# Optimization experiments

Measured on AMD Instinct MI355X. Metric: run time of the kernel, lower is better.

Reference implementation:

```python
import jax, jax.numpy as jnp
import numpy as np

N = 100000   # nodes
E = 1600000  # directed edges
D_IN, D_HID, D_OUT, N_CLS = 128, 256, 128, 10
EPS = 1e-5


def gcn_conv(x, W, b, src, dst, n):
    # PyG GCNConv: h = XW, add self loops, sym-normalize, scatter-add to dst, + bias
    h = x @ W
    loop = jnp.arange(n)
    src_f = jnp.concatenate([src, loop])
    dst_f = jnp.concatenate([dst, loop])
    deg = jax.ops.segment_sum(jnp.ones(src_f.shape[0], h.dtype), dst_f, num_segments=n)
    dinv = jnp.where(deg > 0, jax.lax.rsqrt(deg), jnp.zeros_like(deg))
    norm = dinv[src_f] * dinv[dst_f]                    # [E+N]
    out = jax.ops.segment_sum(h[src_f] * norm[:, None], dst_f, num_segments=n)
    return out + b


def batchnorm(x, gamma, beta):
    # training-mode BatchNorm1d (batch statistics, biased variance)
    mu = x.mean(0)
    var = x.var(0)
    return gamma * (x - mu) * jax.lax.rsqrt(var + EPS) + beta


def setup_inputs() -> dict:
    key = jax.random.key(0)
    ks = jax.random.split(key, 12)
    x = jax.random.normal(ks[0], (N, D_IN), jnp.float32)
    edge_index = jax.random.randint(ks[1], (2, E), 0, N, dtype=jnp.int64)
    def lin(k, fi, fo):
        s = 1.0 / np.sqrt(fi)
        return jax.random.uniform(k, (fi, fo), jnp.float32, -s, s)
    return {
        "x": x, "edge_index": edge_index,
        "W1": lin(ks[2], D_IN, D_HID), "b1": jnp.zeros(D_HID, jnp.float32),
        "g1": jnp.ones(D_HID, jnp.float32), "beta1": jnp.zeros(D_HID, jnp.float32),
        "W2": lin(ks[3], D_HID, D_HID), "b2": jnp.zeros(D_HID, jnp.float32),
        "g2": jnp.ones(D_HID, jnp.float32), "beta2": jnp.zeros(D_HID, jnp.float32),
        "W3": lin(ks[4], D_HID, D_OUT), "b3": jnp.zeros(D_OUT, jnp.float32),
        "g3": jnp.ones(D_OUT, jnp.float32), "beta3": jnp.zeros(D_OUT, jnp.float32),
        "Wout": lin(ks[5], D_OUT, N_CLS), "bout": jnp.zeros(N_CLS, jnp.float32),
    }


def reference(x, edge_index, W1, b1, g1, beta1, W2, b2, g2, beta2,
              W3, b3, g3, beta3, Wout, bout):
    src, dst = edge_index[0], edge_index[1]
    h = jax.nn.relu(batchnorm(gcn_conv(x, W1, b1, src, dst, N), g1, beta1))
    h = jax.nn.relu(batchnorm(gcn_conv(h, W2, b2, src, dst, N), g2, beta2))
    h = jax.nn.relu(batchnorm(gcn_conv(h, W3, b3, src, dst, N), g3, beta3))
    return h @ Wout + bout
```

## Files before the change

### kernel.cpp

```cpp
#include <hip/hip_runtime.h>
#include <hip/hip_fp16.h>
#include <cstdint>
#include <cstddef>

#define EPS_BN 1e-5f
#define NSLICE 16

static inline int cdiv(int a, int b) { return (a + b - 1) / b; }

using half8   = __attribute__((ext_vector_type(8))) _Float16;
using floatx4 = __attribute__((ext_vector_type(4))) float;

__device__ __forceinline__ float atomAddF(float* p, float v) {
    return unsafeAtomicAdd(p, v);
}


__global__ __launch_bounds__(256) void k_hist(const int* __restrict__ dst, int E,
                                              int NBLK, int NBUCK, int* __restrict__ H) {
    __shared__ int h[256];
    int t = threadIdx.x;
    h[t] = 0;
    __syncthreads();
    int base = blockIdx.x * 4096;
#pragma unroll
    for (int j = 0; j < 16; ++j) {
        int e = base + j * 256 + t;
        if (e < E) atomicAdd(&h[dst[e] >> 9], 1);
    }
    __syncthreads();
    if (t < NBUCK) H[t * NBLK + blockIdx.x] = h[t];
}

__global__ __launch_bounds__(256) void k_scan_reduce(const int* __restrict__ in, int m,
                                                     int* __restrict__ bsum) {
    int base = blockIdx.x * 1024;
    int t = threadIdx.x;
    int s = 0;
#pragma unroll
    for (int i = 0; i < 4; ++i) {
        int idx = base + t * 4 + i;
        if (idx < m) s += in[idx];
    }
    __shared__ int sm[256];
    sm[t] = s;
    __syncthreads();
    for (int off = 128; off > 0; off >>= 1) {
        if (t < off) sm[t] += sm[t + off];
        __syncthreads();
    }
    if (t == 0) bsum[blockIdx.x] = sm[0];
}

__global__ void k_scan_bsum(int* __restrict__ bsum, int nb) {
    if (threadIdx.x == 0 && blockIdx.x == 0) {
        int acc = 0;
        for (int i = 0; i < nb; ++i) { int v = bsum[i]; bsum[i] = acc; acc += v; }
    }
}

__global__ __launch_bounds__(256) void k_scan_final(const int* __restrict__ in, int m,
                                                    const int* __restrict__ bsum,
                                                    int* __restrict__ outS) {
    int base = blockIdx.x * 1024;
    int t = threadIdx.x;
    int v[4];
    int s = 0;
#pragma unroll
    for (int i = 0; i < 4; ++i) {
        int idx = base + t * 4 + i;
        v[i] = (idx < m) ? in[idx] : 0;
        s += v[i];
    }
    __shared__ int sm[256];
    sm[t] = s;
    __syncthreads();
    for (int off = 1; off < 256; off <<= 1) {
        int x = (t >= off) ? sm[t - off] : 0;
        __syncthreads();
        sm[t] += x;
        __syncthreads();
    }
    int excl = sm[t] - s + bsum[blockIdx.x];
#pragma unroll
    for (int i = 0; i < 4; ++i) {
        int idx = base + t * 4 + i;
        if (idx < m) { outS[idx] = excl; excl += v[i]; }
    }
}

__global__ __launch_bounds__(256) void k_bucket(const int* __restrict__ src,
                                                const int* __restrict__ dst, int E,
                                                int NBLK, int NBUCK,
                                                const int* __restrict__ S,
                                                unsigned* __restrict__ pairs) {
    __shared__ int cur[256];
    int t = threadIdx.x;
    if (t < NBUCK) cur[t] = S[t * NBLK + blockIdx.x];
    __syncthreads();
    int base = blockIdx.x * 4096;
#pragma unroll
    for (int j = 0; j < 16; ++j) {
        int e = base + j * 256 + t;
        if (e < E) {
            unsigned s = (unsigned)src[e];
            unsigned d = (unsigned)dst[e];
            int p = atomicAdd(&cur[d >> 9], 1);
            pairs[p] = ((d & 511u) << 17) | s;
        }
    }
}

__global__ __launch_bounds__(256) void k_build(const unsigned* __restrict__ pairs,
                                               const int* __restrict__ S,
                                               int NBLK, int NBUCK, int n, int E,
                                               int* __restrict__ endoff,
                                               float* __restrict__ dinv,
                                               int* __restrict__ csr) {
    int b = blockIdx.x;
    int nbase = b << 9;
    int bstart = S[b * NBLK];
    int bend = (b == NBUCK - 1) ? E : S[(b + 1) * NBLK];
    int t = threadIdx.x;
    __shared__ int sdeg[512];
    __shared__ int scur[512];
    __shared__ int stmp[256];
    sdeg[t] = 0; sdeg[t + 256] = 0;
    __syncthreads();
    for (int e = bstart + t; e < bend; e += 256)
        atomicAdd(&sdeg[pairs[e] >> 17], 1);
    __syncthreads();
    int d0 = sdeg[2 * t], d1 = sdeg[2 * t + 1];
    int ps = d0 + d1;
    stmp[t] = ps;
    __syncthreads();
    for (int off = 1; off < 256; off <<= 1) {
        int x = (t >= off) ? stmp[t - off] : 0;
        __syncthreads();
        stmp[t] += x;
        __syncthreads();
    }
    int c0 = bstart + stmp[t] - ps;
    int c1 = c0 + d0;
    scur[2 * t] = c0;
    scur[2 * t + 1] = c1;
    int v0 = nbase + 2 * t, v1 = v0 + 1;
    if (v0 < n) { endoff[v0] = c1;      dinv[v0] = rsqrtf((float)(d0 + 1)); }
    if (v1 < n) { endoff[v1] = c1 + d1; dinv[v1] = rsqrtf((float)(d1 + 1)); }
    __syncthreads();
    for (int e = bstart + t; e < bend; e += 256) {
        unsigned p = pairs[e];
        int pos = atomicAdd(&scur[p >> 17], 1);
        csr[pos] = (int)(p & 0x1FFFFu);
    }
}

__global__ __launch_bounds__(256) void k_wtall(const float* __restrict__ W1,
                                               const float* __restrict__ W2,
                                               const float* __restrict__ W3,
                                               __half* __restrict__ Wt1,
                                               __half* __restrict__ Wt2,
                                               __half* __restrict__ Wt3) {
    int idx = blockIdx.x * 256 + threadIdx.x;
    if (idx < 32768) {
        int k = idx >> 8, c = idx & 255;
        Wt1[c * 128 + k] = __float2half(W1[idx]);
    } else if (idx < 98304) {
        int r = idx - 32768;
        int k = r >> 8, c = r & 255;
        Wt2[c * 256 + k] = __float2half(W2[r]);
    } else if (idx < 131072) {
        int r = idx - 98304;
        int k = r >> 7, c = r & 127;
        Wt3[c * 256 + k] = __float2half(W3[r]);
    }
}

__global__ __launch_bounds__(256) void k_x2h(const float* __restrict__ x,
                                             const float* __restrict__ dinv,
                                             __half* __restrict__ xh, int n) {
    int idx = blockIdx.x * 256 + threadIdx.x;
    int total = n * 16;
    if (idx >= total) return;
    int row = idx >> 4;
    float dv = dinv[row];
    const float4* p = (const float4*)x + (size_t)idx * 2;
    float4 a = p[0], b = p[1];
    uint4 o; __half2* oh = (__half2*)&o;
    oh[0] = __floats2half2_rn(a.x * dv, a.y * dv);
    oh[1] = __floats2half2_rn(a.z * dv, a.w * dv);
    oh[2] = __floats2half2_rn(b.x * dv, b.y * dv);
    oh[3] = __floats2half2_rn(b.z * dv, b.w * dv);
    ((uint4*)xh)[idx] = o;
}

__device__ __forceinline__ void acc8(float* acc, uint4 d) {
    const __half2* h = (const __half2*)&d;
#pragma unroll
    for (int j = 0; j < 4; ++j) {
        float2 f = __half22float2(h[j]);
        acc[2 * j] += f.x; acc[2 * j + 1] += f.y;
    }
}

template<int D, bool STATS>
__global__ __launch_bounds__(256) void k_gather_h(const int* __restrict__ csr,
                                                  const int* __restrict__ endoff,
                                                  const __half* __restrict__ P,
                                                  const float* __restrict__ dinv,
                                                  __half* __restrict__ S, int n,
                                                  float* __restrict__ sums,
                                                  float* __restrict__ sqs) {
    constexpr int LPN = D / 8;
    constexpr int NPB = 256 / LPN;
    __shared__ float red[STATS ? 2048 : 1];
    int t = threadIdx.x;
    int lane = t % LPN;
    int sub = t / LPN;
    float sacc[8] = {}, sqacc[8] = {};
    for (int vb = blockIdx.x * NPB; vb < n; vb += gridDim.x * NPB) {
        int v = vb + sub;
        if (v >= n) continue;
        int beg = (v == 0) ? 0 : endoff[v - 1];
        int end = endoff[v];
        float acc[8];
        {
            uint4 d = *((const uint4*)(P + (size_t)v * D) + lane);
            const __half2* h = (const __half2*)&d;
#pragma unroll
            for (int j = 0; j < 4; ++j) {
                float2 f = __half22float2(h[j]);
                acc[2 * j] = f.x; acc[2 * j + 1] = f.y;
            }
        }
        int i = beg;
        int rem = (end - beg) & 7;
        if (rem & 4) {
            uint4 dd[4];
#pragma unroll
            for (int u = 0; u < 4; ++u)
                dd[u] = *((const uint4*)(P + (size_t)csr[i + u] * D) + lane);
#pragma unroll
            for (int u = 0; u < 4; ++u) acc8(acc, dd[u]);
            i += 4;
        }
        if (rem & 2) {
            uint4 d0 = *((const uint4*)(P + (size_t)csr[i] * D) + lane);
            uint4 d1 = *((const uint4*)(P + (size_t)csr[i + 1] * D) + lane);
            acc8(acc, d0); acc8(acc, d1);
            i += 2;
        }
        if (rem & 1) {
            uint4 d0 = *((const uint4*)(P + (size_t)csr[i] * D) + lane);
            acc8(acc, d0);
            i += 1;
        }
        if (i < end) {
            uint4 a[8];
#pragma unroll
            for (int u = 0; u < 8; ++u)
                a[u] = *((const uint4*)(P + (size_t)csr[i + u] * D) + lane);
            for (i += 8; i < end; i += 8) {
                uint4 b[8];
#pragma unroll
                for (int u = 0; u < 8; ++u)
                    b[u] = *((const uint4*)(P + (size_t)csr[i + u] * D) + lane);
#pragma unroll
                for (int u = 0; u < 8; ++u) acc8(acc, a[u]);
#pragma unroll
                for (int u = 0; u < 8; ++u) a[u] = b[u];
            }
#pragma unroll
            for (int u = 0; u < 8; ++u) acc8(acc, a[u]);
        }
        float dv = dinv[v];
        uint4 o; __half2* oh = (__half2*)&o;
#pragma unroll
        for (int j = 0; j < 4; ++j) {
            float a0 = acc[2 * j] * dv, a1 = acc[2 * j + 1] * dv;
            oh[j] = __floats2half2_rn(a0, a1);
            if (STATS) {
                sacc[2 * j] += a0;  sqacc[2 * j] += a0 * a0;
                sacc[2 * j + 1] += a1; sqacc[2 * j + 1] += a1 * a1;
            }
        }
        *((uint4*)(S + (size_t)v * D) + lane) = o;
    }
    if (STATS) {
        int slice = blockIdx.x & (NSLICE - 1);
#pragma unroll
        for (int j = 0; j < 8; ++j) red[t * 8 + j] = sacc[j];
        __syncthreads();
        if (t < D) {
            int lc = t >> 3, j = t & 7;
            float ts = 0.f;
#pragma unroll
            for (int s = 0; s < NPB; ++s) ts += red[(s * LPN + lc) * 8 + j];
            atomAddF(&sums[slice * 256 + t], ts);
        }
        __syncthreads();
#pragma unroll
        for (int j = 0; j < 8; ++j) red[t * 8 + j] = sqacc[j];
        __syncthreads();
        if (t < D) {
            int lc = t >> 3, j = t & 7;
            float tq = 0.f;
#pragma unroll
            for (int s = 0; s < NPB; ++s) tq += red[(s * LPN + lc) * 8 + j];
            atomAddF(&sqs[slice * 256 + t], tq);
        }
    }
}

template<int K, int NC, bool SCALE, bool BNIN, bool STATS>
__global__ __launch_bounds__(256) void k_gemm_mfma(const __half* __restrict__ A,
                                                   const __half* __restrict__ Wt,
                                                   const float* __restrict__ dinv,
                                                   const float* __restrict__ isum,
                                                   const float* __restrict__ isq,
                                                   const float* __restrict__ g,
                                                   const float* __restrict__ beta,
                                                   float* __restrict__ osum,
                                                   float* __restrict__ osq,
                                                   __half* __restrict__ C, int n) {
    constexpr int LDA = 40;
    __shared__ _Float16 As[128 * LDA];
    __shared__ _Float16 Bs[128 * LDA];
    __shared__ float ssc[BNIN ? K : 1];
    __shared__ float ssh[BNIN ? K : 1];
    __shared__ float scs[STATS ? 128 : 1];
    __shared__ float scq[STATS ? 128 : 1];
    int tid = threadIdx.x;
    if (BNIN) {
        float nf = (float)n;
        for (int i = tid; i < K; i += 256) {
            float su = 0.f, sq = 0.f;
#pragma unroll
            for (int s = 0; s < NSLICE; ++s) {
                su += isum[s * 256 + i];
                sq += isq[s * 256 + i];
            }
            float mu = su / nf;
            float var = sq / nf - mu * mu;
            float sc = g[i] * rsqrtf(var + EPS_BN);
            ssc[i] = sc; ssh[i] = beta[i] - mu * sc;
        }
        __syncthreads();
    }
    int wave = tid >> 6, lane = tid & 63;
    int q = lane >> 4, l16 = lane & 15;
    int row0 = blockIdx.x * 128;
    int col0 = blockIdx.y * 128;
    floatx4 acc[2][8];
#pragma unroll
    for (int r = 0; r < 2; ++r)
#pragma unroll
        for (int c = 0; c < 8; ++c) acc[r][c] = (floatx4)0.0f;

    for (int k0 = 0; k0 < K; k0 += 32) {
#pragma unroll
        for (int i = 0; i < 2; ++i) {
            int s = tid + i * 256;
            int r = s >> 2, ks = s & 3;
            uint4 d = *(const uint4*)(A + (size_t)(row0 + r) * K + k0 + ks * 8);
            if (BNIN) {
                const __half2* h = (const __half2*)&d;
                uint4 o; __half2* oh = (__half2*)&o;
                int kb = k0 + ks * 8;
#pragma unroll
                for (int j = 0; j < 4; ++j) {
                    float2 f = __half22float2(h[j]);
                    float y0 = fmaxf(0.f, f.x * ssc[kb + 2 * j]     + ssh[kb + 2 * j]);
                    float y1 = fmaxf(0.f, f.y * ssc[kb + 2 * j + 1] + ssh[kb + 2 * j + 1]);
                    oh[j] = __floats2half2_rn(y0, y1);
                }
                d = o;
            }
            *(uint4*)&As[r * LDA + ks * 8] = d;
        }
#pragma unroll
        for (int i = 0; i < 2; ++i) {
            int s = tid + i * 256;
            int r = s >> 2, ks = s & 3;
            uint4 d = *(const uint4*)(Wt + (size_t)(col0 + r) * K + k0 + ks * 8);
            *(uint4*)&Bs[r * LDA + ks * 8] = d;
        }
        __syncthreads();
        half8 bf[8];
#pragma unroll
        for (int c = 0; c < 8; ++c)
            bf[c] = *(const half8*)&Bs[(c * 16 + l16) * LDA + q * 8];
#pragma unroll
        for (int r = 0; r < 2; ++r) {
            half8 af = *(const half8*)&As[(wave * 32 + r * 16 + l16) * LDA + q * 8];
#pragma unroll
            for (int c = 0; c < 8; ++c)
                acc[r][c] = __builtin_amdgcn_mfma_f32_16x16x32_f16(af, bf[c], acc[r][c], 0, 0, 0);
        }
        __syncthreads();
    }
    float colsum[8] = {};
    float colsq[8]  = {};
#pragma unroll
    for (int r = 0; r < 2; ++r) {
#pragma unroll
        for (int reg = 0; reg < 4; ++reg) {
            int grow = row0 + wave * 32 + r * 16 + q * 4 + reg;
            float sc = 1.f;
            if (SCALE) sc = (grow < n) ? dinv[grow] : 0.f;
            __half* cp = C + (size_t)grow * NC + col0 + l16;
#pragma unroll
            for (int c = 0; c < 8; ++c) {
                float v = acc[r][c][reg] * sc;
                cp[c * 16] = __float2half(v);
                if (STATS && grow < n) { colsum[c] += v; colsq[c] += v * v; }
            }
        }
    }
    if (STATS) {
        if (tid < 128) { scs[tid] = 0.f; scq[tid] = 0.f; }
        __syncthreads();
#pragma unroll
        for (int c = 0; c < 8; ++c) {
            atomicAdd(&scs[c * 16 + l16], colsum[c]);
            atomicAdd(&scq[c * 16 + l16], colsq[c]);
        }
        __syncthreads();
        if (tid < 128) {
            int slice = blockIdx.x & (NSLICE - 1);
            atomAddF(&osum[slice * 256 + col0 + tid], scs[tid]);
            atomAddF(&osq[slice * 256 + col0 + tid], scq[tid]);
        }
    }
}

__global__ __launch_bounds__(256) void k_out(const __half* __restrict__ H,
                                             const float* __restrict__ sums,
                                             const float* __restrict__ sqs,
                                             const float* __restrict__ g,
                                             const float* __restrict__ beta,
                                             const float* __restrict__ Wout,
                                             const float* __restrict__ bout,
                                             float* __restrict__ out, int n) {
    __shared__ float Wl[128 * 10];
    __shared__ float bl[10];
    __shared__ float osc[128];
    __shared__ float osh[128];
    __shared__ float red[64 * 40];
    int tid = threadIdx.x;
    for (int i = tid; i < 1280; i += 256) Wl[i] = Wout[i];
    if (tid < 10) bl[tid] = bout[tid];
    if (tid < 128) {
        float nf = (float)n;
        float su = 0.f, sq = 0.f;
#pragma unroll
        for (int s = 0; s < NSLICE; ++s) {
            su += sums[s * 256 + tid];
            sq += sqs[s * 256 + tid];
        }
        float mu = su / nf;
        float var = sq / nf - mu * mu;
        float sc = g[tid] * rsqrtf(var + EPS_BN);
        osc[tid] = sc; osh[tid] = beta[tid] - mu * sc;
    }
    __syncthreads();
    int rl = tid >> 2;
    int q = tid & 3;
    int r = blockIdx.x * 64 + rl;
    float p[10] = {};
    if (r < n) {
        const __half* a = H + (size_t)r * 128 + q * 32;
#pragma unroll 8
        for (int k = 0; k < 32; ++k) {
            int col = q * 32 + k;
            float av = fmaxf(0.f, __half2float(a[k]) * osc[col] + osh[col]);
            const float* wr = Wl + col * 10;
#pragma unroll
            for (int c = 0; c < 10; ++c) p[c] += av * wr[c];
        }
    }
    float* rr = red + (size_t)(rl * 4 + q) * 10;
#pragma unroll
    for (int c = 0; c < 10; ++c) rr[c] = p[c];
    __syncthreads();
    if (q == 0 && r < n) {
        const float* rb = red + (size_t)rl * 40;
#pragma unroll
        for (int c = 0; c < 10; ++c) {
            out[(size_t)r * 10 + c] = rb[c] + rb[10 + c] + rb[20 + c] + rb[30 + c] + bl[c];
        }
    }
}

extern "C" void kernel_launch(void* const* d_in, const int* in_sizes, int n_in,
                              void* d_out, int out_size, void* d_ws, size_t ws_size,
                              hipStream_t stream) {
    const float* x    = (const float*)d_in[0];
    const int*   ei   = (const int*)d_in[1];
    const float* W1   = (const float*)d_in[2];
    const float* g1   = (const float*)d_in[4];
    const float* be1  = (const float*)d_in[5];
    const float* W2   = (const float*)d_in[6];
    const float* g2   = (const float*)d_in[8];
    const float* be2  = (const float*)d_in[9];
    const float* W3   = (const float*)d_in[10];
    const float* g3   = (const float*)d_in[12];
    const float* be3  = (const float*)d_in[13];
    const float* Wout = (const float*)d_in[14];
    const float* bout = (const float*)d_in[15];
    float* out = (float*)d_out;

    int n = in_sizes[0] / 128;
    int E = in_sizes[1] / 2;
    const int* esrc = ei;
    const int* edst = ei + E;
    int npad = cdiv(n, 128) * 128;
    int NBLK = cdiv(E, 4096);
    int NBUCK = (n + 511) >> 9;
    if (NBUCK > 256) return;
    int m = NBUCK * NBLK;
    int nb2 = cdiv(m, 1024);

    const size_t align = 256;
    auto al = [&](size_t s) { return (s + align - 1) & ~(align - 1); };
    size_t n4 = al((size_t)n * 4 + 512);

    const size_t statsLayer = (size_t)NSLICE * 256 * 2 * 4;
    const size_t statsTotal = statsLayer * 3;

    char* ws = (char*)d_ws;
    size_t o_end   = 0;
    size_t o_dinv  = o_end + n4;
    size_t o_stats = o_dinv + n4;
    size_t o_bsum  = o_stats + statsTotal;
    size_t o_H     = o_bsum + 1024;
    size_t o_Hs    = o_H + al((size_t)m * 4);
    size_t o_csr   = o_Hs + al((size_t)m * 4);
    size_t o_pairs = o_csr + al((size_t)E * 4);
    size_t o_w1    = o_pairs + al((size_t)E * 4);
    size_t o_w2    = o_w1 + al(256 * 128 * 2);
    size_t o_w3    = o_w2 + al(256 * 256 * 2);
    size_t o_A128a = o_w3 + al(128 * 256 * 2);
    size_t o_A128b = o_A128a + al((size_t)npad * 128 * 2);
    size_t o_A256a = o_A128b + al((size_t)npad * 128 * 2);
    size_t o_A256b = o_A256a + al((size_t)npad * 256 * 2);
    size_t need    = o_A256b + (size_t)npad * 256 * 2;
    if (ws_size < need) return;

    int*      endoff = (int*)(ws + o_end);
    float*    dinv   = (float*)(ws + o_dinv);
    float*    sums1  = (float*)(ws + o_stats);
    float*    sqs1   = sums1 + NSLICE * 256;
    float*    sums2  = (float*)(ws + o_stats + statsLayer);
    float*    sqs2   = sums2 + NSLICE * 256;
    float*    sums3  = (float*)(ws + o_stats + 2 * statsLayer);
    float*    sqs3   = sums3 + NSLICE * 256;
    int*      bsum   = (int*)(ws + o_bsum);
    int*      H      = (int*)(ws + o_H);
    int*      Hs     = (int*)(ws + o_Hs);
    int*      csr    = (int*)(ws + o_csr);
    unsigned* pairs  = (unsigned*)(ws + o_pairs);
    __half*   Wt1    = (__half*)(ws + o_w1);
    __half*   Wt2    = (__half*)(ws + o_w2);
    __half*   Wt3    = (__half*)(ws + o_w3);
    __half*   xh     = (__half*)(ws + o_A128a);
    __half*   S3     = (__half*)(ws + o_A128a);
    __half*   G1     = (__half*)(ws + o_A128b);
    __half*   P3     = (__half*)(ws + o_A128b);
    __half*   P1     = (__half*)(ws + o_A256a);
    __half*   S2     = (__half*)(ws + o_A256a);
    __half*   P2     = (__half*)(ws + o_A256b);

    hipMemsetAsync((void*)sums1, 0, statsTotal, stream);
    k_hist<<<NBLK, 256, 0, stream>>>(edst, E, NBLK, NBUCK, H);
    k_scan_reduce<<<nb2, 256, 0, stream>>>(H, m, bsum);
    k_scan_bsum<<<1, 64, 0, stream>>>(bsum, nb2);
    k_scan_final<<<nb2, 256, 0, stream>>>(H, m, bsum, Hs);
    k_bucket<<<NBLK, 256, 0, stream>>>(esrc, edst, E, NBLK, NBUCK, Hs, pairs);
    k_build<<<NBUCK, 256, 0, stream>>>(pairs, Hs, NBLK, NBUCK, n, E, endoff, dinv, csr);

    k_wtall<<<cdiv(131072, 256), 256, 0, stream>>>(W1, W2, W3, Wt1, Wt2, Wt3);

    k_x2h<<<cdiv(n * 16, 256), 256, 0, stream>>>(x, dinv, xh, n);

    k_gather_h<128, false><<<cdiv(n, 16), 256, 0, stream>>>(
        csr, endoff, xh, dinv, G1, n, nullptr, nullptr);
    k_gemm_mfma<128, 256, false, false, true><<<dim3(npad / 128, 2), 256, 0, stream>>>(
        G1, Wt1, dinv, nullptr, nullptr, nullptr, nullptr, sums1, sqs1, P1, n);

    k_gemm_mfma<256, 256, true, true, false><<<dim3(npad / 128, 2), 256, 0, stream>>>(
        P1, Wt2, dinv, sums1, sqs1, g1, be1, nullptr, nullptr, P2, n);
    k_gather_h<256, true><<<cdiv(n, 8), 256, 0, stream>>>(
        csr, endoff, P2, dinv, S2, n, sums2, sqs2);

    k_gemm_mfma<256, 128, true, true, false><<<dim3(npad / 128, 1), 256, 0, stream>>>(
        S2, Wt3, dinv, sums2, sqs2, g2, be2, nullptr, nullptr, P3, n);
    k_gather_h<128, true><<<cdiv(n, 16), 256, 0, stream>>>(
        csr, endoff, P3, dinv, S3, n, sums3, sqs3);

    k_out<<<cdiv(n, 64), 256, 0, stream>>>(S3, sums3, sqs3, g3, be3, Wout, bout, out, n);
}
```

Measured before the change: 585.9 us.

## Fuse prep kernels with stats zeroing, retile MFMA waves, widen output rows

```diff
diff --git a/kernel.cpp b/kernel.cpp
--- a/kernel.cpp
+++ b/kernel.cpp
@@ -155,43 +155,46 @@
     }
 }
 
-__global__ __launch_bounds__(256) void k_wtall(const float* __restrict__ W1,
-                                               const float* __restrict__ W2,
-                                               const float* __restrict__ W3,
-                                               __half* __restrict__ Wt1,
-                                               __half* __restrict__ Wt2,
-                                               __half* __restrict__ Wt3) {
+__global__ __launch_bounds__(256) void k_prep(const float* __restrict__ x,
+                                              const float* __restrict__ dinv,
+                                              const float* __restrict__ W1,
+                                              const float* __restrict__ W2,
+                                              const float* __restrict__ W3,
+                                              __half* __restrict__ xh,
+                                              __half* __restrict__ Wt1,
+                                              __half* __restrict__ Wt2,
+                                              __half* __restrict__ Wt3,
+                                              float* __restrict__ stats, int n) {
     int idx = blockIdx.x * 256 + threadIdx.x;
-    if (idx < 32768) {
-        int k = idx >> 8, c = idx & 255;
-        Wt1[c * 128 + k] = __float2half(W1[idx]);
-    } else if (idx < 98304) {
-        int r = idx - 32768;
+    int nx = n * 16;
+    if (idx < nx) {
+        int row = idx >> 4;
+        float dv = dinv[row];
+        const float4* p = (const float4*)x + (size_t)idx * 2;
+        float4 a = p[0], b = p[1];
+        uint4 o; __half2* oh = (__half2*)&o;
+        oh[0] = __floats2half2_rn(a.x * dv, a.y * dv);
+        oh[1] = __floats2half2_rn(a.z * dv, a.w * dv);
+        oh[2] = __floats2half2_rn(b.x * dv, b.y * dv);
+        oh[3] = __floats2half2_rn(b.z * dv, b.w * dv);
+        ((uint4*)xh)[idx] = o;
+        return;
+    }
+    int r = idx - nx;
+    if (r < 32768) {
         int k = r >> 8, c = r & 255;
-        Wt2[c * 256 + k] = __float2half(W2[r]);
-    } else if (idx < 131072) {
-        int r = idx - 98304;
-        int k = r >> 7, c = r & 127;
-        Wt3[c * 256 + k] = __float2half(W3[r]);
-    }
-}
-
-__global__ __launch_bounds__(256) void k_x2h(const float* __restrict__ x,
-                                             const float* __restrict__ dinv,
-                                             __half* __restrict__ xh, int n) {
-    int idx = blockIdx.x * 256 + threadIdx.x;
-    int total = n * 16;
-    if (idx >= total) return;
-    int row = idx >> 4;
-    float dv = dinv[row];
-    const float4* p = (const float4*)x + (size_t)idx * 2;
-    float4 a = p[0], b = p[1];
-    uint4 o; __half2* oh = (__half2*)&o;
-    oh[0] = __floats2half2_rn(a.x * dv, a.y * dv);
-    oh[1] = __floats2half2_rn(a.z * dv, a.w * dv);
-    oh[2] = __floats2half2_rn(b.x * dv, b.y * dv);
-    oh[3] = __floats2half2_rn(b.z * dv, b.w * dv);
-    ((uint4*)xh)[idx] = o;
+        Wt1[c * 128 + k] = __float2half(W1[r]);
+    } else if (r < 98304) {
+        int r2 = r - 32768;
+        int k = r2 >> 8, c = r2 & 255;
+        Wt2[c * 256 + k] = __float2half(W2[r2]);
+    } else if (r < 131072) {
+        int r2 = r - 98304;
+        int k = r2 >> 7, c = r2 & 127;
+        Wt3[c * 256 + k] = __float2half(W3[r2]);
+    } else if (r < 131072 + NSLICE * 256 * 6) {
+        stats[r - 131072] = 0.f;
+    }
 }
 
 __device__ __forceinline__ void acc8(float* acc, uint4 d) {
@@ -348,14 +351,15 @@
         __syncthreads();
     }
     int wave = tid >> 6, lane = tid & 63;
+    int wr = wave >> 1, wc = wave & 1;
     int q = lane >> 4, l16 = lane & 15;
     int row0 = blockIdx.x * 128;
     int col0 = blockIdx.y * 128;
-    floatx4 acc[2][8];
-#pragma unroll
-    for (int r = 0; r < 2; ++r)
-#pragma unroll
-        for (int c = 0; c < 8; ++c) acc[r][c] = (floatx4)0.0f;
+    floatx4 acc[4][4];
+#pragma unroll
+    for (int r = 0; r < 4; ++r)
+#pragma unroll
+        for (int c = 0; c < 4; ++c) acc[r][c] = (floatx4)0.0f;
 
     for (int k0 = 0; k0 < K; k0 += 32) {
 #pragma unroll
@@ -386,31 +390,32 @@
             *(uint4*)&Bs[r * LDA + ks * 8] = d;
         }
         __syncthreads();
-        half8 bf[8];
-#pragma unroll
-        for (int c = 0; c < 8; ++c)
-            bf[c] = *(const half8*)&Bs[(c * 16 + l16) * LDA + q * 8];
-#pragma unroll
-        for (int r = 0; r < 2; ++r) {
-            half8 af = *(const half8*)&As[(wave * 32 + r * 16 + l16) * LDA + q * 8];
-#pragma unroll
-            for (int c = 0; c < 8; ++c)
-                acc[r][c] = __builtin_amdgcn_mfma_f32_16x16x32_f16(af, bf[c], acc[r][c], 0, 0, 0);
-        }
-        __syncthreads();
-    }
-    float colsum[8] = {};
-    float colsq[8]  = {};
-#pragma unroll
-    for (int r = 0; r < 2; ++r) {
+        half8 af[4], bf[4];
+#pragma unroll
+        for (int r = 0; r < 4; ++r)
+            af[r] = *(const half8*)&As[(wr * 64 + r * 16 + l16) * LDA + q * 8];
+#pragma unroll
+        for (int c = 0; c < 4; ++c)
+            bf[c] = *(const half8*)&Bs[(wc * 64 + c * 16 + l16) * LDA + q * 8];
+#pragma unroll
+        for (int r = 0; r < 4; ++r)
+#pragma unroll
+            for (int c = 0; c < 4; ++c)
+                acc[r][c] = __builtin_amdgcn_mfma_f32_16x16x32_f16(af[r], bf[c], acc[r][c], 0, 0, 0);
+        __syncthreads();
+    }
+    float colsum[4] = {};
+    float colsq[4]  = {};
+#pragma unroll
+    for (int r = 0; r < 4; ++r) {
 #pragma unroll
         for (int reg = 0; reg < 4; ++reg) {
-            int grow = row0 + wave * 32 + r * 16 + q * 4 + reg;
+            int grow = row0 + wr * 64 + r * 16 + q * 4 + reg;
             float sc = 1.f;
             if (SCALE) sc = (grow < n) ? dinv[grow] : 0.f;
-            __half* cp = C + (size_t)grow * NC + col0 + l16;
-#pragma unroll
-            for (int c = 0; c < 8; ++c) {
+            __half* cp = C + (size_t)grow * NC + col0 + wc * 64 + l16;
+#pragma unroll
+            for (int c = 0; c < 4; ++c) {
                 float v = acc[r][c][reg] * sc;
                 cp[c * 16] = __float2half(v);
                 if (STATS && grow < n) { colsum[c] += v; colsq[c] += v * v; }
@@ -421,9 +426,9 @@
         if (tid < 128) { scs[tid] = 0.f; scq[tid] = 0.f; }
         __syncthreads();
 #pragma unroll
-        for (int c = 0; c < 8; ++c) {
-            atomicAdd(&scs[c * 16 + l16], colsum[c]);
-            atomicAdd(&scq[c * 16 + l16], colsq[c]);
+        for (int c = 0; c < 4; ++c) {
+            atomicAdd(&scs[wc * 64 + c * 16 + l16], colsum[c]);
+            atomicAdd(&scq[wc * 64 + c * 16 + l16], colsq[c]);
         }
         __syncthreads();
         if (tid < 128) {
@@ -446,7 +451,7 @@
     __shared__ float bl[10];
     __shared__ float osc[128];
     __shared__ float osh[128];
-    __shared__ float red[64 * 40];
+    __shared__ float red[256 * 10];
     int tid = threadIdx.x;
     for (int i = tid; i < 1280; i += 256) Wl[i] = Wout[i];
     if (tid < 10) bl[tid] = bout[tid];
@@ -464,30 +469,30 @@
         osc[tid] = sc; osh[tid] = beta[tid] - mu * sc;
     }
     __syncthreads();
-    int rl = tid >> 2;
-    int q = tid & 3;
-    int r = blockIdx.x * 64 + rl;
+    int rl = tid >> 1;
+    int h2 = tid & 1;
+    int r = blockIdx.x * 128 + rl;
     float p[10] = {};
     if (r < n) {
-        const __half* a = H + (size_t)r * 128 + q * 32;
+        const __half* a = H + (size_t)r * 128 + h2 * 64;
 #pragma unroll 8
-        for (int k = 0; k < 32; ++k) {
-            int col = q * 32 + k;
+        for (int k = 0; k < 64; ++k) {
+            int col = h2 * 64 + k;
             float av = fmaxf(0.f, __half2float(a[k]) * osc[col] + osh[col]);
             const float* wr = Wl + col * 10;
 #pragma unroll
             for (int c = 0; c < 10; ++c) p[c] += av * wr[c];
         }
     }
-    float* rr = red + (size_t)(rl * 4 + q) * 10;
+    float* rr = red + (size_t)tid * 10;
 #pragma unroll
     for (int c = 0; c < 10; ++c) rr[c] = p[c];
     __syncthreads();
-    if (q == 0 && r < n) {
-        const float* rb = red + (size_t)rl * 40;
+    if (h2 == 0 && r < n) {
+        const float* rb = red + (size_t)tid * 10;
 #pragma unroll
         for (int c = 0; c < 10; ++c) {
-            out[(size_t)r * 10 + c] = rb[c] + rb[10 + c] + rb[20 + c] + rb[30 + c] + bl[c];
+            out[(size_t)r * 10 + c] = rb[c] + rb[10 + c] + bl[c];
         }
     }
 }
@@ -549,7 +554,8 @@
 
     int*      endoff = (int*)(ws + o_end);
     float*    dinv   = (float*)(ws + o_dinv);
-    float*    sums1  = (float*)(ws + o_stats);
+    float*    stats  = (float*)(ws + o_stats);
+    float*    sums1  = stats;
     float*    sqs1   = sums1 + NSLICE * 256;
     float*    sums2  = (float*)(ws + o_stats + statsLayer);
     float*    sqs2   = sums2 + NSLICE * 256;
@@ -571,7 +577,6 @@
     __half*   S2     = (__half*)(ws + o_A256a);
     __half*   P2     = (__half*)(ws + o_A256b);
 
-    hipMemsetAsync((void*)sums1, 0, statsTotal, stream);
     k_hist<<<NBLK, 256, 0, stream>>>(edst, E, NBLK, NBUCK, H);
     k_scan_reduce<<<nb2, 256, 0, stream>>>(H, m, bsum);
     k_scan_bsum<<<1, 64, 0, stream>>>(bsum, nb2);
@@ -579,9 +584,9 @@
     k_bucket<<<NBLK, 256, 0, stream>>>(esrc, edst, E, NBLK, NBUCK, Hs, pairs);
     k_build<<<NBUCK, 256, 0, stream>>>(pairs, Hs, NBLK, NBUCK, n, E, endoff, dinv, csr);
 
-    k_wtall<<<cdiv(131072, 256), 256, 0, stream>>>(W1, W2, W3, Wt1, Wt2, Wt3);
-
-    k_x2h<<<cdiv(n * 16, 256), 256, 0, stream>>>(x, dinv, xh, n);
+    int prepTotal = n * 16 + 131072 + NSLICE * 256 * 6;
+    k_prep<<<cdiv(prepTotal, 256), 256, 0, stream>>>(
+        x, dinv, W1, W2, W3, xh, Wt1, Wt2, Wt3, stats, n);
 
     k_gather_h<128, false><<<cdiv(n, 16), 256, 0, stream>>>(
         csr, endoff, xh, dinv, G1, n, nullptr, nullptr);
@@ -598,5 +603,5 @@
     k_gather_h<128, true><<<cdiv(n, 16), 256, 0, stream>>>(
         csr, endoff, P3, dinv, S3, n, sums3, sqs3);
 
-    k_out<<<cdiv(n, 64), 256, 0, stream>>>(S3, sums3, sqs3, g3, be3, Wout, bout, out, n);
-}
+    k_out<<<cdiv(n, 128), 256, 0, stream>>>(S3, sums3, sqs3, g3, be3, Wout, bout, out, n);
+}
```

Result: faster. 568.5 us, median of 2 (-3.0%).
